# Optimization experiments

Hardware: AMD Instinct MI355X
Metric: run time of the kernel (lower is better)

## Reference

```python
import jax, jax.numpy as jnp
import numpy as np

N_HEADS, D_MODEL, DK, DV = 16, 1024, 64, 64
B, S = 4, 2048


def setup_inputs() -> dict:
    key = jax.random.key(0)
    ks = jax.random.split(key, 7)
    scale = 1.0 / np.sqrt(D_MODEL)
    return {
        "Q": jax.random.normal(ks[0], (B, S, D_MODEL), dtype=jnp.float32),
        "K": jax.random.normal(ks[1], (B, S, D_MODEL), dtype=jnp.float32),
        "V": jax.random.normal(ks[2], (B, S, D_MODEL), dtype=jnp.float32),
        # Linear weights stored as [in, out] so y = x @ W (equivalent to torch x @ W.T)
        "w_q": jax.random.normal(ks[3], (D_MODEL, N_HEADS * DK), dtype=jnp.float32) * scale,
        "w_k": jax.random.normal(ks[4], (D_MODEL, N_HEADS * DK), dtype=jnp.float32) * scale,
        "w_v": jax.random.normal(ks[5], (D_MODEL, N_HEADS * DV), dtype=jnp.float32) * scale,
        "w_o": jax.random.normal(ks[6], (N_HEADS * DV, D_MODEL), dtype=jnp.float32) * scale,
    }


def reference(Q, K, V, w_q, w_k, w_v, w_o):
    b, s, _ = Q.shape
    # projections -> [B, H, S, d]
    q = (Q @ w_q).reshape(b, s, N_HEADS, DK).transpose(0, 2, 1, 3)
    k = (K @ w_k).reshape(b, s, N_HEADS, DK).transpose(0, 2, 1, 3)
    v = (V @ w_v).reshape(b, s, N_HEADS, DV).transpose(0, 2, 1, 3)
    # scaled dot-product attention, full [B,H,S,S] scores (matches source)
    scores = jnp.einsum("bhqd,bhkd->bhqk", q, k) / jnp.sqrt(jnp.float32(DK))
    attn = jax.nn.softmax(scores, axis=-1)
    x = jnp.einsum("bhqk,bhkd->bhqd", attn, v)
    x = x.transpose(0, 2, 1, 3).reshape(b, s, N_HEADS * DV)
    return x @ w_o
```

## Files before the change

kernel.cpp:

```cpp
#include <hip/hip_runtime.h>
#include <stdint.h>

#define B_   4
#define S_   2048
#define H_   16
#define D_   64
#define DM_  1024
#define NTOK (B_ * S_)

typedef __attribute__((ext_vector_type(8))) short short8;
typedef __attribute__((ext_vector_type(4))) float floatx4;

__device__ inline unsigned short f2bf(float f) {
  unsigned int u = __float_as_uint(f);
  u += 0x7FFFu + ((u >> 16) & 1u);
  return (unsigned short)(u >> 16);
}

__device__ inline floatx4 mfma_bf16(short8 a, short8 b, floatx4 c) {
  return __builtin_amdgcn_mfma_f32_16x16x32_bf16(a, b, c, 0, 0, 0);
}

__device__ inline unsigned int pack_bf2(float lo, float hi) {
  return __builtin_amdgcn_perm(__float_as_uint(hi), __float_as_uint(lo), 0x07060302u);
}

__device__ inline void gload_lds16(const unsigned short* g, unsigned short* l) {
  __builtin_amdgcn_global_load_lds(
      (const __attribute__((address_space(1))) unsigned int*)g,
      (__attribute__((address_space(3))) unsigned int*)l, 16, 0, 0);
}

__global__ __launch_bounds__(256) void cast_bf16_kernel(const float* __restrict__ in,
                                                        unsigned short* __restrict__ out,
                                                        int n4) {
  int i = blockIdx.x * 256 + threadIdx.x;
  if (i < n4) {
    float4 v = ((const float4*)in)[i];
    ushort4 o;
    o.x = f2bf(v.x); o.y = f2bf(v.y); o.z = f2bf(v.z); o.w = f2bf(v.w);
    ((ushort4*)out)[i] = o;
  }
}

__global__ __launch_bounds__(256) void wt_kernel(const float* __restrict__ w0,
                                                 const float* __restrict__ w1,
                                                 const float* __restrict__ w2,
                                                 const float* __restrict__ w3,
                                                 unsigned short* __restrict__ o0,
                                                 unsigned short* __restrict__ o1,
                                                 unsigned short* __restrict__ o2,
                                                 unsigned short* __restrict__ o3) {
  __shared__ unsigned short T[64 * 68];
  const float* w = blockIdx.z == 0 ? w0 : blockIdx.z == 1 ? w1 : blockIdx.z == 2 ? w2 : w3;
  unsigned short* o = blockIdx.z == 0 ? o0 : blockIdx.z == 1 ? o1 : blockIdx.z == 2 ? o2 : o3;
  const int tid = threadIdx.x;
  const int R0 = blockIdx.y * 64;
  const int C0 = blockIdx.x * 64;
  for (int it = 0; it < 16; it++) {
    int lr = it * 4 + (tid >> 6), lc = tid & 63;
    T[lc * 68 + lr] = f2bf(w[(size_t)(R0 + lr) * 1024 + C0 + lc]);
  }
  __syncthreads();
  for (int it = 0; it < 2; it++) {
    int orow = it * 32 + (tid >> 3), oc = (tid & 7) * 8;
    union { ushort4 h[2]; short8 v8; } u;
    u.h[0] = *(const ushort4*)(T + orow * 68 + oc);
    u.h[1] = *(const ushort4*)(T + orow * 68 + oc + 4);
    *(short8*)(o + (size_t)(C0 + orow) * 1024 + R0 + oc) = u.v8;
  }
}

template <int MODE>
__global__ __launch_bounds__(256) void gemm_bt_kernel(const unsigned short* __restrict__ A,
                                                      const unsigned short* __restrict__ BT,
                                                      void* __restrict__ Cout,
                                                      float scale) {
  constexpr int K = 1024;
  __shared__ unsigned short As[128 * 32];
  __shared__ unsigned short Bs[128 * 32];

  const int tid  = threadIdx.x;
  const int wave = tid >> 6, lane = tid & 63;
  const int quad = lane >> 4, l16 = lane & 15;
  const int wm = wave >> 1, wn = wave & 1;
  const int m0 = blockIdx.y * 128, n0 = blockIdx.x * 128;

  floatx4 acc[4][4] = {};

  for (int k0 = 0; k0 < K; k0 += 32) {
    for (int p = 0; p < 2; p++) {
      int i = p * 256 + wave * 64 + lane;
      int row = i >> 2, c = i & 3;
      gload_lds16(A  + (size_t)(m0 + row) * K + k0 + c * 8,
                  As + (size_t)(p * 256 + wave * 64) * 8);
      gload_lds16(BT + (size_t)(n0 + row) * K + k0 + c * 8,
                  Bs + (size_t)(p * 256 + wave * 64) * 8);
    }
    __syncthreads();

    short8 af[4], bfr[4];
    for (int f = 0; f < 4; f++) {
      af[f]  = *(const short8*)(As + (wm * 64 + f * 16 + l16) * 32 + quad * 8);
      bfr[f] = *(const short8*)(Bs + (wn * 64 + f * 16 + l16) * 32 + quad * 8);
    }
    for (int fm = 0; fm < 4; fm++)
      for (int fn = 0; fn < 4; fn++)
        acc[fm][fn] = mfma_bf16(af[fm], bfr[fn], acc[fm][fn]);
    __syncthreads();
  }

  for (int fm = 0; fm < 4; fm++)
    for (int fn = 0; fn < 4; fn++)
      for (int r = 0; r < 4; r++) {
        int gm = m0 + wm * 64 + fm * 16 + quad * 4 + r;
        int gn = n0 + wn * 64 + fn * 16 + l16;
        float val = acc[fm][fn][r] * scale;
        if (MODE == 0) {
          int b = gm >> 11, s = gm & 2047;
          int h = gn >> 6,  d = gn & 63;
          ((unsigned short*)Cout)[((size_t)((b * H_ + h) * S_ + s) << 6) + d] = f2bf(val);
        } else if (MODE == 1) {
          ((float*)Cout)[((size_t)gm << 10) + gn] = val;
        } else {
          int b = gm >> 11, s = gm & 2047;
          int h = gn >> 6,  d = gn & 63;
          int p = ((s & 63) >> 4) + (s & 15) * 4;
          ((unsigned short*)Cout)[(((size_t)(b * H_ + h) * 64 + d) << 11) + (s & ~63) + p] = f2bf(val);
        }
      }
}

__global__ __launch_bounds__(256, 2) void attn_kernel(const unsigned short* __restrict__ q,
                                                      const unsigned short* __restrict__ k,
                                                      const unsigned short* __restrict__ vT,
                                                      unsigned short* __restrict__ X) {
  __shared__ unsigned short Ks[64 * 64];
  __shared__ unsigned short Vt[64 * 64];
  __shared__ unsigned short Ps[4][16 * 72];

  const int tid  = threadIdx.x;
  const int wave = tid >> 6, lane = tid & 63;
  const int quad = lane >> 4, l16 = lane & 15;
  const int bh = blockIdx.y;
  const int q0 = blockIdx.x * 256;

  const unsigned short* qh = q  + (size_t)bh * S_ * 64;
  const unsigned short* kh = k  + (size_t)bh * S_ * 64;
  const unsigned short* vh = vT + (size_t)bh * 64 * S_;

  short8 qf[4][2];
  for (int qt = 0; qt < 4; qt++) {
    int row = q0 + wave * 64 + qt * 16 + l16;
    for (int kk = 0; kk < 2; kk++)
      qf[qt][kk] = *(const short8*)(qh + (size_t)row * 64 + kk * 32 + quad * 8);
  }

  short8 onesb = {};
  if (l16 == 0)
    for (int e = 0; e < 8; e++) onesb[e] = (short)0x3F80;

  floatx4 O[4][4] = {};
  floatx4 lacc[4] = {};

  for (int j0 = 0; j0 < S_; j0 += 64) {
    __syncthreads();

    for (int p = 0; p < 2; p++) {
      int i = p * 256 + tid;
      int r = i >> 3;
      int gc = (i & 7) ^ (r & 7);
      gload_lds16(kh + (size_t)(j0 + r) * 64 + gc * 8,
                  Ks + (size_t)(p * 256 + wave * 64) * 8);
      gload_lds16(vh + (size_t)r * S_ + j0 + gc * 8,
                  Vt + (size_t)(p * 256 + wave * 64) * 8);
    }
    __syncthreads();

    short8 kf[4][2];
    for (int jf = 0; jf < 4; jf++)
      for (int kk = 0; kk < 2; kk++) {
        int sl = (kk * 4 + quad) ^ (l16 & 7);
        kf[jf][kk] = *(const short8*)(Ks + (jf * 16 + l16) * 64 + sl * 8);
      }
    short8 vf[4][2];
    for (int df = 0; df < 4; df++)
      for (int jk = 0; jk < 2; jk++) {
        int sl = (jk * 4 + quad) ^ (l16 & 7);
        vf[df][jk] = *(const short8*)(Vt + (df * 16 + l16) * 64 + sl * 8);
      }

    unsigned short* pw = Ps[wave];
    for (int qt = 0; qt < 4; qt++) {
      floatx4 s[4] = {};
      for (int jf = 0; jf < 4; jf++) {
        s[jf] = mfma_bf16(qf[qt][0], kf[jf][0], s[jf]);
        s[jf] = mfma_bf16(qf[qt][1], kf[jf][1], s[jf]);
      }
      for (int r = 0; r < 4; r++) {
        float e0 = exp2f(s[0][r]), e1 = exp2f(s[1][r]);
        float e2 = exp2f(s[2][r]), e3 = exp2f(s[3][r]);
        uint2 pk;
        pk.x = pack_bf2(e0, e1);
        pk.y = pack_bf2(e2, e3);
        *(uint2*)(pw + (quad * 4 + r) * 72 + l16 * 4) = pk;
      }
      short8 pa0 = *(const short8*)(pw + l16 * 72 + quad * 8);
      short8 pa1 = *(const short8*)(pw + l16 * 72 + 32 + quad * 8);
      lacc[qt] = mfma_bf16(pa0, onesb, lacc[qt]);
      lacc[qt] = mfma_bf16(pa1, onesb, lacc[qt]);
      for (int df = 0; df < 4; df++) {
        O[qt][df] = mfma_bf16(pa0, vf[df][0], O[qt][df]);
        O[qt][df] = mfma_bf16(pa1, vf[df][1], O[qt][df]);
      }
    }
  }

  const int b = bh >> 4, h = bh & 15;
  for (int qt = 0; qt < 4; qt++)
    for (int r = 0; r < 4; r++) {
      float lsum = __shfl(lacc[qt][r], (lane & 48));
      float inv = 1.0f / lsum;
      int row = q0 + wave * 64 + qt * 16 + quad * 4 + r;
      unsigned short* dst = X + ((size_t)(b * S_ + row) << 10) + h * 64;
      for (int df = 0; df < 4; df++)
        dst[df * 16 + l16] = f2bf(O[qt][df][r] * inv);
    }
}

extern "C" void kernel_launch(void* const* d_in, const int* in_sizes, int n_in,
                              void* d_out, int out_size, void* d_ws, size_t ws_size,
                              hipStream_t stream) {
  const float* Q  = (const float*)d_in[0];
  const float* K  = (const float*)d_in[1];
  const float* V  = (const float*)d_in[2];
  const float* wq = (const float*)d_in[3];
  const float* wk = (const float*)d_in[4];
  const float* wv = (const float*)d_in[5];
  const float* wo = (const float*)d_in[6];

  char* ws = (char*)d_ws;
  unsigned short* buf0 = (unsigned short*)ws;
  unsigned short* wqT  = (unsigned short*)(ws + (size_t)(16 << 20));
  unsigned short* wkT  = (unsigned short*)(ws + (size_t)(18 << 20));
  unsigned short* wvT  = (unsigned short*)(ws + (size_t)(20 << 20));
  unsigned short* woT  = (unsigned short*)(ws + (size_t)(22 << 20));
  unsigned short* qP   = (unsigned short*)(ws + (size_t)(24 << 20));
  unsigned short* kP   = (unsigned short*)(ws + (size_t)(40 << 20));
  unsigned short* vTg  = (unsigned short*)(ws + (size_t)(56 << 20));

  const int n4 = NTOK * DM_ / 4;
  const float SC = 0.18033688011112043f;

  wt_kernel<<<dim3(16, 16, 4), dim3(256), 0, stream>>>(wq, wk, wv, wo, wqT, wkT, wvT, woT);

  cast_bf16_kernel<<<dim3(8192), dim3(256), 0, stream>>>(Q, buf0, n4);
  gemm_bt_kernel<0><<<dim3(8, 64), dim3(256), 0, stream>>>(buf0, wqT, qP, SC);
  cast_bf16_kernel<<<dim3(8192), dim3(256), 0, stream>>>(K, buf0, n4);
  gemm_bt_kernel<0><<<dim3(8, 64), dim3(256), 0, stream>>>(buf0, wkT, kP, 1.0f);
  cast_bf16_kernel<<<dim3(8192), dim3(256), 0, stream>>>(V, buf0, n4);
  gemm_bt_kernel<2><<<dim3(8, 64), dim3(256), 0, stream>>>(buf0, wvT, vTg, 1.0f);

  attn_kernel<<<dim3(8, 64), dim3(256), 0, stream>>>(qP, kP, vTg, buf0);

  gemm_bt_kernel<1><<<dim3(8, 64), dim3(256), 0, stream>>>(buf0, woT, (float*)d_out, 1.0f);
}
```

Before: 377.7 us.

## Use 8-wave attention blocks with fewer query rows per wave and swizzled block order

The attention kernel now runs 512 threads (8 waves) per block, each wave handling 32 query rows instead of 64. This halves the per-wave O/lacc/qf register state and allows a higher launch-bounds occupancy target. The K/V tile load becomes a single pass per thread. V fragments are loaded on demand inside the PV loop instead of being held for the whole tile. Block indexing is remapped so blocks that share a batch-head run close together, which may improve L2 reuse of K/V. In exchange, the score computation per K tile is split across more waves, which adds LDS traffic for V reads and more barrier participants.

```diff
diff --git a/kernel.cpp b/kernel.cpp
--- a/kernel.cpp
+++ b/kernel.cpp
@@ -131,27 +131,27 @@
       }
 }
 
-__global__ __launch_bounds__(256, 2) void attn_kernel(const unsigned short* __restrict__ q,
+__global__ __launch_bounds__(512, 4) void attn_kernel(const unsigned short* __restrict__ q,
                                                       const unsigned short* __restrict__ k,
                                                       const unsigned short* __restrict__ vT,
                                                       unsigned short* __restrict__ X) {
   __shared__ unsigned short Ks[64 * 64];
   __shared__ unsigned short Vt[64 * 64];
-  __shared__ unsigned short Ps[4][16 * 72];
+  __shared__ unsigned short Ps[8][16 * 72];
 
   const int tid  = threadIdx.x;
   const int wave = tid >> 6, lane = tid & 63;
   const int quad = lane >> 4, l16 = lane & 15;
-  const int bh = blockIdx.y;
-  const int q0 = blockIdx.x * 256;
+  const int bh = blockIdx.x * 8 + (blockIdx.y >> 3);
+  const int q0 = (blockIdx.y & 7) * 256;
 
   const unsigned short* qh = q  + (size_t)bh * S_ * 64;
   const unsigned short* kh = k  + (size_t)bh * S_ * 64;
   const unsigned short* vh = vT + (size_t)bh * 64 * S_;
 
-  short8 qf[4][2];
-  for (int qt = 0; qt < 4; qt++) {
-    int row = q0 + wave * 64 + qt * 16 + l16;
+  short8 qf[2][2];
+  for (int qt = 0; qt < 2; qt++) {
+    int row = q0 + wave * 32 + qt * 16 + l16;
     for (int kk = 0; kk < 2; kk++)
       qf[qt][kk] = *(const short8*)(qh + (size_t)row * 64 + kk * 32 + quad * 8);
   }
@@ -160,20 +160,19 @@
   if (l16 == 0)
     for (int e = 0; e < 8; e++) onesb[e] = (short)0x3F80;
 
-  floatx4 O[4][4] = {};
-  floatx4 lacc[4] = {};
+  floatx4 O[2][4] = {};
+  floatx4 lacc[2] = {};
 
   for (int j0 = 0; j0 < S_; j0 += 64) {
     __syncthreads();
 
-    for (int p = 0; p < 2; p++) {
-      int i = p * 256 + tid;
-      int r = i >> 3;
-      int gc = (i & 7) ^ (r & 7);
+    {
+      int r  = tid >> 3;
+      int gc = (tid & 7) ^ (r & 7);
       gload_lds16(kh + (size_t)(j0 + r) * 64 + gc * 8,
-                  Ks + (size_t)(p * 256 + wave * 64) * 8);
+                  Ks + (size_t)(wave * 64) * 8);
       gload_lds16(vh + (size_t)r * S_ + j0 + gc * 8,
-                  Vt + (size_t)(p * 256 + wave * 64) * 8);
+                  Vt + (size_t)(wave * 64) * 8);
     }
     __syncthreads();
 
@@ -183,15 +182,10 @@
         int sl = (kk * 4 + quad) ^ (l16 & 7);
         kf[jf][kk] = *(const short8*)(Ks + (jf * 16 + l16) * 64 + sl * 8);
       }
-    short8 vf[4][2];
-    for (int df = 0; df < 4; df++)
-      for (int jk = 0; jk < 2; jk++) {
-        int sl = (jk * 4 + quad) ^ (l16 & 7);
-        vf[df][jk] = *(const short8*)(Vt + (df * 16 + l16) * 64 + sl * 8);
-      }
 
     unsigned short* pw = Ps[wave];
-    for (int qt = 0; qt < 4; qt++) {
+    short8 pa[2][2];
+    for (int qt = 0; qt < 2; qt++) {
       floatx4 s[4] = {};
       for (int jf = 0; jf < 4; jf++) {
         s[jf] = mfma_bf16(qf[qt][0], kf[jf][0], s[jf]);
@@ -205,23 +199,30 @@
         pk.y = pack_bf2(e2, e3);
         *(uint2*)(pw + (quad * 4 + r) * 72 + l16 * 4) = pk;
       }
-      short8 pa0 = *(const short8*)(pw + l16 * 72 + quad * 8);
-      short8 pa1 = *(const short8*)(pw + l16 * 72 + 32 + quad * 8);
-      lacc[qt] = mfma_bf16(pa0, onesb, lacc[qt]);
-      lacc[qt] = mfma_bf16(pa1, onesb, lacc[qt]);
-      for (int df = 0; df < 4; df++) {
-        O[qt][df] = mfma_bf16(pa0, vf[df][0], O[qt][df]);
-        O[qt][df] = mfma_bf16(pa1, vf[df][1], O[qt][df]);
+      pa[qt][0] = *(const short8*)(pw + l16 * 72 + quad * 8);
+      pa[qt][1] = *(const short8*)(pw + l16 * 72 + 32 + quad * 8);
+      lacc[qt] = mfma_bf16(pa[qt][0], onesb, lacc[qt]);
+      lacc[qt] = mfma_bf16(pa[qt][1], onesb, lacc[qt]);
+    }
+
+    for (int df = 0; df < 4; df++) {
+      int sl0 = quad ^ (l16 & 7);
+      int sl1 = (4 + quad) ^ (l16 & 7);
+      short8 v0 = *(const short8*)(Vt + (df * 16 + l16) * 64 + sl0 * 8);
+      short8 v1 = *(const short8*)(Vt + (df * 16 + l16) * 64 + sl1 * 8);
+      for (int qt = 0; qt < 2; qt++) {
+        O[qt][df] = mfma_bf16(pa[qt][0], v0, O[qt][df]);
+        O[qt][df] = mfma_bf16(pa[qt][1], v1, O[qt][df]);
       }
     }
   }
 
   const int b = bh >> 4, h = bh & 15;
-  for (int qt = 0; qt < 4; qt++)
+  for (int qt = 0; qt < 2; qt++)
     for (int r = 0; r < 4; r++) {
       float lsum = __shfl(lacc[qt][r], (lane & 48));
       float inv = 1.0f / lsum;
-      int row = q0 + wave * 64 + qt * 16 + quad * 4 + r;
+      int row = q0 + wave * 32 + qt * 16 + quad * 4 + r;
       unsigned short* dst = X + ((size_t)(b * S_ + row) << 10) + h * 64;
       for (int df = 0; df < 4; df++)
         dst[df * 16 + l16] = f2bf(O[qt][df][r] * inv);
@@ -261,7 +262,7 @@
   cast_bf16_kernel<<<dim3(8192), dim3(256), 0, stream>>>(V, buf0, n4);
   gemm_bt_kernel<2><<<dim3(8, 64), dim3(256), 0, stream>>>(buf0, wvT, vTg, 1.0f);
 
-  attn_kernel<<<dim3(8, 64), dim3(256), 0, stream>>>(qP, kP, vTg, buf0);
+  attn_kernel<<<dim3(8, 64), dim3(512), 0, stream>>>(qP, kP, vTg, buf0);
 
   gemm_bt_kernel<1><<<dim3(8, 64), dim3(256), 0, stream>>>(buf0, woT, (float*)d_out, 1.0f);
 }
```

Result: no change. 371.7 us (-1.6%).
